# Kernel optimization log

Measured on AMD Instinct MI355X. Metric: run time of the kernel, lower is better.

The kernel has to match this reference:

```python
import jax, jax.numpy as jnp
import numpy as np

GROUP = 4
BN_EPS = 1e-5


def setup_inputs() -> dict:
    key = jax.random.key(0)
    ks = jax.random.split(key, 6)
    B, C, N = 8, 64, 4096
    K, KS, OUT = 20, 20, 64
    feature = jax.random.normal(ks[0], (B, C, N), dtype=jnp.float32)
    neigh_indexs = jax.random.randint(ks[1], (B * N, K), 0, B * N, dtype=jnp.int64)
    permatrix = jax.random.normal(ks[2], (B * N, K, KS), dtype=jnp.float32)
    conv_w = jax.random.normal(ks[3], (OUT, C), dtype=jnp.float32) * (1.0 / np.sqrt(C))
    conv_b = jax.random.normal(ks[4], (OUT,), dtype=jnp.float32) * 0.01
    bn_w = jnp.ones((OUT,), dtype=jnp.float32)
    bn_b = jnp.zeros((OUT,), dtype=jnp.float32)
    return {"feature": feature, "neigh_indexs": neigh_indexs, "permatrix": permatrix,
            "conv_w": conv_w, "conv_b": conv_b, "bn_w": bn_w, "bn_b": bn_b}


def reference(feature, neigh_indexs, permatrix, conv_w, conv_b, bn_w, bn_b):
    B, C, N = feature.shape
    BN = B * N
    K = neigh_indexs.shape[1]
    # flatten points: [B, C, N] -> [B*N, C]
    flat = jnp.transpose(feature, (0, 2, 1)).reshape(BN, C)
    # irregular neighbor gather: [B*N, k, C] -> [B*N, C, k]
    feats = jnp.transpose(flat[neigh_indexs], (0, 2, 1))
    # group channel shuffle (num_feat > 3 path)
    feats = feats.reshape(BN, GROUP, C // GROUP, K)
    feats = jnp.transpose(feats, (0, 2, 1, 3)).reshape(BN, C, K)
    # per-point soft-permutation matmul: [B*N, C, kernel_size]
    feats = jnp.einsum('nck,nks->ncs', feats, permatrix)
    # conv1x1 (in_c -> out_c) then max over kernel_size
    out = jnp.einsum('ncs,oc->nos', feats, conv_w) + conv_b[None, :, None]
    out = jnp.max(out, axis=-1)  # [B*N, out_c]
    out = jnp.transpose(out.reshape(B, N, -1), (0, 2, 1))  # [B, out_c, N]
    # BatchNorm1d (training-mode batch statistics over batch+points)
    mean = jnp.mean(out, axis=(0, 2), keepdims=True)
    var = jnp.var(out, axis=(0, 2), keepdims=True)
    out = (out - mean) * jax.lax.rsqrt(var + BN_EPS)
    return out * bn_w[None, :, None] + bn_b[None, :, None]
```

## Files before the change

kernel.cpp:

```cpp
#include <hip/hip_runtime.h>

#define B_SZ 8
#define C_IN 64
#define N_PT 4096
#define BN_TOT 32768
#define KNB 20
#define KSZ 20
#define C_OUT 64
#define BN_EPS 1e-5f

__global__ void k0_prep(const float* __restrict__ conv_w,
                        float* __restrict__ w2t,
                        float* __restrict__ sums ) {
    int t = threadIdx.x;
    for (int i = t; i < C_IN * C_OUT; i += 256) {
        int c = i >> 6, o = i & 63;
        int cs = ((c & 15) << 2) | (c >> 4);
        w2t[c * 64 + o] = conv_w[o * 64 + cs];
    }
    if (t < 128) sums[t] = 0.f;
}

__global__ __launch_bounds__(256) void k1_gemm(const float* __restrict__ feat,
                                               const float* __restrict__ w2t,
                                               float* __restrict__ G) {
    __shared__ float fl[C_IN * 64];
    const int b  = blockIdx.x >> 6;
    const int n0 = (blockIdx.x & 63) << 6;
    const int t  = threadIdx.x;

    const float4* fsrc = reinterpret_cast<const float4*>(
        feat + (size_t)b * C_IN * N_PT + n0);
    float4* fl4 = reinterpret_cast<float4*>(fl);
#pragma unroll
    for (int j = 0; j < 4; ++j) {
        int idx = j * 256 + t;
        int c = idx >> 4, p4 = idx & 15;
        fl4[idx] = fsrc[c * (N_PT / 4) + p4];
    }
    __syncthreads();

    const int lane = t & 63;
    const int ob = __builtin_amdgcn_readfirstlane((t >> 6) << 4);

    float acc[16];
#pragma unroll
    for (int j = 0; j < 16; ++j) acc[j] = 0.f;

#pragma unroll 8
    for (int c = 0; c < C_IN; ++c) {
        float fc = fl[c * 64 + lane];
        const float* wrow = w2t + c * 64 + ob;
#pragma unroll
        for (int j = 0; j < 16; ++j) acc[j] += fc * wrow[j];
    }

    size_t m = (size_t)b * N_PT + n0 + lane;
    float4* gdst = reinterpret_cast<float4*>(G + m * 64 + ob);
#pragma unroll
    for (int j = 0; j < 4; ++j)
        gdst[j] = make_float4(acc[4 * j], acc[4 * j + 1],
                              acc[4 * j + 2], acc[4 * j + 3]);
}

__global__ __launch_bounds__(256) void k2_main(const int* __restrict__ nidx,
                                               const float* __restrict__ P,
                                               const float* __restrict__ G,
                                               const float* __restrict__ conv_b,
                                               float* __restrict__ omax,
                                               float* __restrict__ sums) {
    const int t = threadIdx.x;
    const int lane = t & 63;
    const int wid = t >> 6;
    const int gw = blockIdx.x * 4 + wid;
    const float cb = conv_b[lane];
    float ls = 0.f, ls2 = 0.f;

    for (int i = 0; i < 8; ++i) {
        const int n = __builtin_amdgcn_readfirstlane(gw * 8 + i);

        const int* ip = nidx + (size_t)n * KNB;
        float g[KNB];
#pragma unroll
        for (int k = 0; k < KNB; ++k) {
            int m = ip[k];
            g[k] = G[(size_t)m * 64 + lane];
        }

        float acc[KSZ];
#pragma unroll
        for (int s = 0; s < KSZ; ++s) acc[s] = 0.f;

        const float* pp = P + (size_t)n * (KNB * KSZ);
#pragma unroll
        for (int k = 0; k < KNB; ++k) {
#pragma unroll
            for (int s = 0; s < KSZ; ++s)
                acc[s] += g[k] * pp[k * KSZ + s];
        }

        float mx = acc[0];
#pragma unroll
        for (int s = 1; s < KSZ; ++s) mx = fmaxf(mx, acc[s]);
        mx += cb;
        omax[(size_t)n * 64 + lane] = mx;
        ls += mx;
        ls2 += mx * mx;
    }

    __shared__ float r1[4][64], r2[4][64];
    r1[wid][lane] = ls;
    r2[wid][lane] = ls2;
    __syncthreads();
    if (wid == 0) {
        float a = r1[0][lane] + r1[1][lane] + r1[2][lane] + r1[3][lane];
        float c2 = r2[0][lane] + r2[1][lane] + r2[2][lane] + r2[3][lane];
        atomicAdd(&sums[lane], a);
        atomicAdd(&sums[64 + lane], c2);
    }
}

__global__ void k3_stats(const float* __restrict__ sums,
                         const float* __restrict__ bn_w,
                         const float* __restrict__ bn_b,
                         float* __restrict__ ss) {
    int o = threadIdx.x;
    const float inv = 1.f / (float)BN_TOT;
    float mean = sums[o] * inv;
    float var = sums[64 + o] * inv - mean * mean;
    float rstd = rsqrtf(var + BN_EPS);
    float sc = rstd * bn_w[o];
    ss[o] = sc;
    ss[64 + o] = bn_b[o] - mean * sc;
}

__global__ __launch_bounds__(256) void k4_apply(const float* __restrict__ omax,
                                                const float* __restrict__ ss,
                                                float* __restrict__ out) {
    const int b  = blockIdx.x >> 6;
    const int n0 = (blockIdx.x & 63) << 6;
    const int t  = threadIdx.x;
    const int nl = t & 63;
    const int ob = __builtin_amdgcn_readfirstlane((t >> 6) << 4);

    const size_t m = (size_t)b * N_PT + n0 + nl;
    const float4* src = reinterpret_cast<const float4*>(omax + m * 64 + ob);
    float v[16];
#pragma unroll
    for (int j = 0; j < 4; ++j) {
        float4 x = src[j];
        v[4 * j] = x.x; v[4 * j + 1] = x.y; v[4 * j + 2] = x.z; v[4 * j + 3] = x.w;
    }
#pragma unroll
    for (int j = 0; j < 16; ++j) {
        int o = ob + j;
        float sc = ss[o];
        float sh = ss[64 + o];
        out[(size_t)b * C_OUT * N_PT + (size_t)o * N_PT + n0 + nl] =
            v[j] * sc + sh;
    }
}

extern "C" void kernel_launch(void* const* d_in, const int* in_sizes, int n_in,
                              void* d_out, int out_size, void* d_ws, size_t ws_size,
                              hipStream_t stream) {
    const float* feature = (const float*)d_in[0];
    const int*   nidx    = (const int*)d_in[1];
    const float* perm    = (const float*)d_in[2];
    const float* conv_w  = (const float*)d_in[3];
    const float* conv_b  = (const float*)d_in[4];
    const float* bn_w    = (const float*)d_in[5];
    const float* bn_b    = (const float*)d_in[6];
    float* out = (float*)d_out;

    char* ws = (char*)d_ws;
    float* G    = (float*)ws;
    float* OM   = (float*)(ws + (size_t)8 * 1024 * 1024);
    float* W2T  = (float*)(ws + (size_t)16 * 1024 * 1024);
    float* SUMS = W2T + 4096;
    float* SS   = SUMS + 128;

    k0_prep<<<1, 256, 0, stream>>>(conv_w, W2T, SUMS);
    k1_gemm<<<512, 256, 0, stream>>>(feature, W2T, G);
    k2_main<<<1024, 256, 0, stream>>>(nidx, perm, G, conv_b, OM, SUMS);
    k3_stats<<<1, 64, 0, stream>>>(SUMS, bn_w, bn_b, SS);
    k4_apply<<<512, 256, 0, stream>>>(OM, SS, out);
}
```

Before: 180.7 us.

## Fuse BN stats into main kernel via last-block counter; widen blocks and grids

Drops the separate stats kernel: the last block of the main gather kernel, found through an atomic counter, computes the BN scale and shift. The main kernel now handles 4 points per wavefront instead of 8, doubling the grid to 2048 blocks, and declares an occupancy hint of 8 blocks per CU. The weight-prep kernel is spread over 16 blocks, and the GEMM and apply kernels use 512 threads with 8 outputs per wave. This removes one launch and adds parallelism, at the cost of an extra atomic counter and a fence in every block.

```diff
diff --git a/kernel.cpp b/kernel.cpp
--- a/kernel.cpp
+++ b/kernel.cpp
@@ -12,16 +12,15 @@
 __global__ void k0_prep(const float* __restrict__ conv_w,
                         float* __restrict__ w2t,
                         float* __restrict__ sums ) {
-    int t = threadIdx.x;
-    for (int i = t; i < C_IN * C_OUT; i += 256) {
-        int c = i >> 6, o = i & 63;
-        int cs = ((c & 15) << 2) | (c >> 4);
-        w2t[c * 64 + o] = conv_w[o * 64 + cs];
-    }
-    if (t < 128) sums[t] = 0.f;
+    int i = blockIdx.x * 256 + threadIdx.x;
+    float v = conv_w[i];
+    int o = i >> 6, co = i & 63;
+    int cn = ((co & 3) << 4) | (co >> 2);
+    w2t[cn * 64 + o] = v;
+    if (blockIdx.x == 0 && threadIdx.x < 132) sums[threadIdx.x] = 0.f;
 }
 
-__global__ __launch_bounds__(256) void k1_gemm(const float* __restrict__ feat,
+__global__ __launch_bounds__(512) void k1_gemm(const float* __restrict__ feat,
                                                const float* __restrict__ w2t,
                                                float* __restrict__ G) {
     __shared__ float fl[C_IN * 64];
@@ -33,42 +32,45 @@
         feat + (size_t)b * C_IN * N_PT + n0);
     float4* fl4 = reinterpret_cast<float4*>(fl);
 #pragma unroll
-    for (int j = 0; j < 4; ++j) {
-        int idx = j * 256 + t;
+    for (int j = 0; j < 2; ++j) {
+        int idx = j * 512 + t;
         int c = idx >> 4, p4 = idx & 15;
         fl4[idx] = fsrc[c * (N_PT / 4) + p4];
     }
     __syncthreads();
 
     const int lane = t & 63;
-    const int ob = __builtin_amdgcn_readfirstlane((t >> 6) << 4);
+    const int ob = __builtin_amdgcn_readfirstlane((t >> 6) << 3);
 
-    float acc[16];
+    float acc[8];
 #pragma unroll
-    for (int j = 0; j < 16; ++j) acc[j] = 0.f;
+    for (int j = 0; j < 8; ++j) acc[j] = 0.f;
 
 #pragma unroll 8
     for (int c = 0; c < C_IN; ++c) {
         float fc = fl[c * 64 + lane];
         const float* wrow = w2t + c * 64 + ob;
 #pragma unroll
-        for (int j = 0; j < 16; ++j) acc[j] += fc * wrow[j];
+        for (int j = 0; j < 8; ++j) acc[j] += fc * wrow[j];
     }
 
     size_t m = (size_t)b * N_PT + n0 + lane;
     float4* gdst = reinterpret_cast<float4*>(G + m * 64 + ob);
-#pragma unroll
-    for (int j = 0; j < 4; ++j)
-        gdst[j] = make_float4(acc[4 * j], acc[4 * j + 1],
-                              acc[4 * j + 2], acc[4 * j + 3]);
+    gdst[0] = make_float4(acc[0], acc[1], acc[2], acc[3]);
+    gdst[1] = make_float4(acc[4], acc[5], acc[6], acc[7]);
 }
 
-__global__ __launch_bounds__(256) void k2_main(const int* __restrict__ nidx,
-                                               const float* __restrict__ P,
-                                               const float* __restrict__ G,
-                                               const float* __restrict__ conv_b,
-                                               float* __restrict__ omax,
-                                               float* __restrict__ sums) {
+__global__ __launch_bounds__(256, 8) void k2_main(
+        const int* __restrict__ nidx,
+        const float* __restrict__ P,
+        const float* __restrict__ G,
+        const float* __restrict__ conv_b,
+        float* __restrict__ omax,
+        float* __restrict__ sums,
+        unsigned* __restrict__ ctr,
+        const float* __restrict__ bn_w,
+        const float* __restrict__ bn_b,
+        float* __restrict__ ss) {
     const int t = threadIdx.x;
     const int lane = t & 63;
     const int wid = t >> 6;
@@ -76,8 +78,9 @@
     const float cb = conv_b[lane];
     float ls = 0.f, ls2 = 0.f;
 
-    for (int i = 0; i < 8; ++i) {
-        const int n = __builtin_amdgcn_readfirstlane(gw * 8 + i);
+#pragma unroll 1
+    for (int i = 0; i < 4; ++i) {
+        const int n = __builtin_amdgcn_readfirstlane(gw * 4 + i);
 
         const int* ip = nidx + (size_t)n * KNB;
         float g[KNB];
@@ -113,46 +116,49 @@
     r2[wid][lane] = ls2;
     __syncthreads();
     if (wid == 0) {
-        float a = r1[0][lane] + r1[1][lane] + r1[2][lane] + r1[3][lane];
+        float a  = r1[0][lane] + r1[1][lane] + r1[2][lane] + r1[3][lane];
         float c2 = r2[0][lane] + r2[1][lane] + r2[2][lane] + r2[3][lane];
         atomicAdd(&sums[lane], a);
         atomicAdd(&sums[64 + lane], c2);
     }
+    __syncthreads();
+
+    __shared__ bool lastBlk;
+    if (t == 0) {
+        __threadfence();
+        lastBlk = (atomicAdd(ctr, 1u) == (unsigned)(gridDim.x - 1));
+    }
+    __syncthreads();
+    if (lastBlk && t < 64) {
+        float s1 = atomicAdd(&sums[t], 0.f);
+        float s2 = atomicAdd(&sums[64 + t], 0.f);
+        const float inv = 1.f / (float)BN_TOT;
+        float mean = s1 * inv;
+        float var  = s2 * inv - mean * mean;
+        float rstd = rsqrtf(var + BN_EPS);
+        float sc = rstd * bn_w[t];
+        ss[t] = sc;
+        ss[64 + t] = bn_b[t] - mean * sc;
+    }
 }
 
-__global__ void k3_stats(const float* __restrict__ sums,
-                         const float* __restrict__ bn_w,
-                         const float* __restrict__ bn_b,
-                         float* __restrict__ ss) {
-    int o = threadIdx.x;
-    const float inv = 1.f / (float)BN_TOT;
-    float mean = sums[o] * inv;
-    float var = sums[64 + o] * inv - mean * mean;
-    float rstd = rsqrtf(var + BN_EPS);
-    float sc = rstd * bn_w[o];
-    ss[o] = sc;
-    ss[64 + o] = bn_b[o] - mean * sc;
-}
-
-__global__ __launch_bounds__(256) void k4_apply(const float* __restrict__ omax,
+__global__ __launch_bounds__(512) void k4_apply(const float* __restrict__ omax,
                                                 const float* __restrict__ ss,
                                                 float* __restrict__ out) {
     const int b  = blockIdx.x >> 6;
     const int n0 = (blockIdx.x & 63) << 6;
     const int t  = threadIdx.x;
     const int nl = t & 63;
-    const int ob = __builtin_amdgcn_readfirstlane((t >> 6) << 4);
+    const int ob = __builtin_amdgcn_readfirstlane((t >> 6) << 3);
 
     const size_t m = (size_t)b * N_PT + n0 + nl;
     const float4* src = reinterpret_cast<const float4*>(omax + m * 64 + ob);
-    float v[16];
+    float v[8];
+    float4 x0 = src[0], x1 = src[1];
+    v[0] = x0.x; v[1] = x0.y; v[2] = x0.z; v[3] = x0.w;
+    v[4] = x1.x; v[5] = x1.y; v[6] = x1.z; v[7] = x1.w;
 #pragma unroll
-    for (int j = 0; j < 4; ++j) {
-        float4 x = src[j];
-        v[4 * j] = x.x; v[4 * j + 1] = x.y; v[4 * j + 2] = x.z; v[4 * j + 3] = x.w;
-    }
-#pragma unroll
-    for (int j = 0; j < 16; ++j) {
+    for (int j = 0; j < 8; ++j) {
         int o = ob + j;
         float sc = ss[o];
         float sh = ss[64 + o];
@@ -178,11 +184,12 @@
     float* OM   = (float*)(ws + (size_t)8 * 1024 * 1024);
     float* W2T  = (float*)(ws + (size_t)16 * 1024 * 1024);
     float* SUMS = W2T + 4096;
-    float* SS   = SUMS + 128;
+    unsigned* CTR = (unsigned*)(SUMS + 128);
+    float* SS   = SUMS + 132;
 
-    k0_prep<<<1, 256, 0, stream>>>(conv_w, W2T, SUMS);
-    k1_gemm<<<512, 256, 0, stream>>>(feature, W2T, G);
-    k2_main<<<1024, 256, 0, stream>>>(nidx, perm, G, conv_b, OM, SUMS);
-    k3_stats<<<1, 64, 0, stream>>>(SUMS, bn_w, bn_b, SS);
-    k4_apply<<<512, 256, 0, stream>>>(OM, SS, out);
+    k0_prep<<<16, 256, 0, stream>>>(conv_w, W2T, SUMS);
+    k1_gemm<<<512, 512, 0, stream>>>(feature, W2T, G);
+    k2_main<<<2048, 256, 0, stream>>>(nidx, perm, G, conv_b, OM, SUMS, CTR,
+                                      bn_w, bn_b, SS);
+    k4_apply<<<512, 512, 0, stream>>>(OM, SS, out);
 }
```

Result: slower. 224.2 us (+24.1%).
